# Optimization experiments

Hardware: AMD Instinct MI355X
Metric: run time of the kernel (lower is better)

Reference implementation:

```python
import jax, jax.numpy as jnp
import numpy as np

IMAGE_SIZE = 224
FMAP_H = FMAP_W = 26   # resnet18 layer2 (28x28) after AvgPool2d(3, stride=1)
N_REWEIGHT = 3
SIGMA = 4.0
KSIZE = 2 * int(4.0 * SIGMA + 0.5) + 1  # 33, kornia-style default kernel for sigma=4


def _gaussian_kernel1d():
    x = np.arange(KSIZE, dtype=np.float64) - (KSIZE - 1) / 2.0
    k = np.exp(-0.5 * (x / SIGMA) ** 2)
    return jnp.asarray((k / k.sum()).astype(np.float32))


def _cdist(x, y):
    # Euclidean cdist: x [N,D], y [M,D] -> [N,M], via the expanded quadratic form.
    x2 = jnp.sum(x * x, axis=1, keepdims=True)          # [N,1]
    y2 = jnp.sum(y * y, axis=1)                          # [M]
    d2 = x2 + y2 - 2.0 * (x @ y.T)                       # [N,M]
    return jnp.sqrt(jnp.maximum(d2, 0.0))


def _gaussian_blur(img):
    # Separable depthwise gaussian blur with reflect padding, img [1,1,H,W].
    k1d = _gaussian_kernel1d()
    pad = (KSIZE - 1) // 2
    x = jnp.pad(img, ((0, 0), (0, 0), (pad, pad), (pad, pad)), mode='reflect')
    kh = k1d.reshape(1, 1, KSIZE, 1)
    kw = k1d.reshape(1, 1, 1, KSIZE)
    dn = ('NCHW', 'OIHW', 'NCHW')
    x = jax.lax.conv_general_dilated(x, kh, (1, 1), 'VALID', dimension_numbers=dn)
    x = jax.lax.conv_general_dilated(x, kw, (1, 1), 'VALID', dimension_numbers=dn)
    return x


def setup_inputs() -> dict:
    key = jax.random.key(0)
    k1, k2 = jax.random.split(key)
    patch = jax.random.normal(k1, (FMAP_H * FMAP_W, 384), dtype=jnp.float32)      # [676, 384]
    patch_lib = jax.random.normal(k2, (100000, 384), dtype=jnp.float32)            # coreset bank
    return {"patch": patch, "patch_lib": patch_lib}


def reference(patch, patch_lib):
    # dist = torch.cdist(patch, patch_lib); min over memory bank
    dist = _cdist(patch, patch_lib)                      # [N, M]
    min_val = jnp.min(dist, axis=1)                      # [N]
    min_idx = jnp.argmin(dist, axis=1)                   # [N]
    s_idx = jnp.argmax(min_val)                          # most anomalous patch
    s_star = min_val[s_idx]
    m_test = patch[s_idx]                                # [D]
    m_star = patch_lib[min_idx[s_idx]]                   # [D]
    # reweighting: k nearest neighbors of m_star in the bank (smallest distances)
    w_dist = jnp.linalg.norm(m_star[None, :] - patch_lib, axis=1)   # [M]
    _, nn_idx = jax.lax.top_k(-w_dist, N_REWEIGHT)                  # indices of k smallest
    m_star_knn = jnp.linalg.norm(m_test[None, :] - patch_lib[nn_idx[1:]], axis=1)  # [k-1]
    D = jnp.sqrt(jnp.asarray(patch.shape[1], dtype=jnp.float32))
    w = 1.0 - jnp.exp(s_star / D) / jnp.sum(jnp.exp(m_star_knn / D))
    s = w * s_star
    # segmentation map: reshape, bilinear upsample (align_corners=False), gaussian blur
    s_map = min_val.reshape(1, 1, FMAP_H, FMAP_W)
    s_map = jax.image.resize(s_map, (1, 1, IMAGE_SIZE, IMAGE_SIZE), method='bilinear')
    s_map = _gaussian_blur(s_map)
    return s, s_map
```

## Files before the change

### kernel.cpp

```cpp
#include <hip/hip_runtime.h>

#define M_PATCH 676
#define K_DIM   384
#define N_LIB   100000
#define BM      128
#define BN      128
#define NCH     782
#define MTILES  6
#define M_PAD   (MTILES*BM)
#define N_PAD   (NCH*BN)
#define XCHUNK  98
#define GRID_GEMM (8*XCHUNK*MTILES)
#define NTOPB   1563
#define NCAND   (NTOPB*3)
#define IMG     224
#define FMAP    26
#define KS      33
#define KHALF   16

typedef __attribute__((ext_vector_type(4))) float  f32x4;
typedef __attribute__((ext_vector_type(8))) short  short8;
typedef unsigned long long ull;

static __device__ __forceinline__ unsigned short f2bf(float f) {
  unsigned u = __float_as_uint(f);
  u = u + 0x7FFFu + ((u >> 16) & 1u);
  return (unsigned short)(u >> 16);
}

static __device__ __forceinline__ ull shfl_xor_u64(ull v, int m) {
  unsigned lo = (unsigned)v, hi = (unsigned)(v >> 32);
  lo = __shfl_xor(lo, m, 64);
  hi = __shfl_xor(hi, m, 64);
  return ((ull)hi << 32) | lo;
}

static __device__ __forceinline__ ull umin64(ull a, ull b) { return a < b ? a : b; }
static __device__ __forceinline__ ull umax64(ull a, ull b) { return a > b ? a : b; }

static __device__ __forceinline__ void gld16(const unsigned short* g, unsigned short* l) {
  __builtin_amdgcn_global_load_lds(
      (const __attribute__((address_space(1))) void*)g,
      (__attribute__((address_space(3))) void*)l, 16, 0, 0);
}

__global__ void pc_norms_cvt_kernel(const float* __restrict__ patch, const float* __restrict__ lib,
                                    float* __restrict__ y2, float* __restrict__ x2,
                                    unsigned short* __restrict__ Abf, unsigned short* __restrict__ Bbf) {
  const int w = threadIdx.x >> 6, lane = threadIdx.x & 63;
  const long r = (long)blockIdx.x * 4 + w;
  if (r < N_PAD) {
    float s;
    if (r < N_LIB) {
      const float2* p = (const float2*)(lib + r * K_DIM);
      ushort2* q = (ushort2*)(Bbf + r * K_DIM);
      float2 v[3];
      s = 0.f;
      #pragma unroll
      for (int j = 0; j < 3; ++j) { v[j] = p[lane + 64 * j]; s += v[j].x * v[j].x + v[j].y * v[j].y; }
      #pragma unroll
      for (int j = 0; j < 3; ++j) q[lane + 64 * j] = make_ushort2(f2bf(v[j].x), f2bf(v[j].y));
      #pragma unroll
      for (int m = 1; m < 64; m <<= 1) s += __shfl_xor(s, m, 64);
    } else {
      s = __builtin_inff();
      ushort2* q = (ushort2*)(Bbf + r * K_DIM);
      #pragma unroll
      for (int j = 0; j < 3; ++j) q[lane + 64 * j] = make_ushort2(0, 0);
    }
    if (lane == 0) y2[r] = s;
  } else {
    const long pr = r - N_PAD;
    if (pr < M_PATCH) {
      const float2* p = (const float2*)(patch + pr * K_DIM);
      ushort2* q = (ushort2*)(Abf + pr * K_DIM);
      float2 v[3]; float s = 0.f;
      #pragma unroll
      for (int j = 0; j < 3; ++j) { v[j] = p[lane + 64 * j]; s += v[j].x * v[j].x + v[j].y * v[j].y; }
      #pragma unroll
      for (int j = 0; j < 3; ++j) q[lane + 64 * j] = make_ushort2(f2bf(v[j].x), f2bf(v[j].y));
      #pragma unroll
      for (int m = 1; m < 64; m <<= 1) s += __shfl_xor(s, m, 64);
      if (lane == 0) x2[pr] = s;
    } else if (pr < M_PAD) {
      ushort2* q = (ushort2*)(Abf + pr * K_DIM);
      #pragma unroll
      for (int j = 0; j < 3; ++j) q[lane + 64 * j] = make_ushort2(0, 0);
    }
  }
}

__launch_bounds__(256, 4)
__global__ void pc_gemm_min_bf16_kernel(const unsigned short* __restrict__ Abf,
                                        const unsigned short* __restrict__ Bbf,
                                        const float* __restrict__ x2g, const float* __restrict__ y2g,
                                        ull* __restrict__ partial) {
  __shared__ unsigned short As[2][BM * 32];
  __shared__ unsigned short Bs[2][BN * 32];
  __shared__ float x2s[BM];
  __shared__ float y2s[BN];
  __shared__ ull red[BM * 2];

  const int l = blockIdx.x;
  const int xcd = l & 7, slot = l >> 3;
  const int chunk = xcd * XCHUNK + slot / MTILES;
  const int mtile = slot % MTILES;
  if (chunk >= NCH) return;

  const int t = threadIdx.x;
  const int m0 = mtile * BM;
  const int n0 = chunk * BN;
  const int wid = t >> 6, lane = t & 63;

  if (t < BM) {
    const int gm = m0 + t;
    x2s[t] = (gm < M_PATCH) ? x2g[gm] : 0.f;
    y2s[t] = y2g[n0 + t];
  }

  const int srow   = (wid << 4) + (lane >> 2);
  const int spiece = (lane & 3) ^ ((lane >> 4) & 3);
  const unsigned short* gA0 = Abf + (size_t)(m0 + srow) * K_DIM + spiece * 8;
  const unsigned short* gA1 = gA0 + (size_t)64 * K_DIM;
  const unsigned short* gB0 = Bbf + (size_t)(n0 + srow) * K_DIM + spiece * 8;
  const unsigned short* gB1 = gB0 + (size_t)64 * K_DIM;

  f32x4 acc[4][4];
  #pragma unroll
  for (int i = 0; i < 4; ++i)
    #pragma unroll
    for (int j = 0; j < 4; ++j) acc[i][j] = (f32x4){0.f, 0.f, 0.f, 0.f};

  const int wm = wid >> 1, wn = wid & 1;
  const int quad = lane >> 4, l15 = lane & 15;
  const int poff = (quad ^ ((l15 >> 2) & 3)) * 8;

  for (int ks = 0; ks < K_DIM / 64; ++ks) {
    __syncthreads();
    #pragma unroll
    for (int h = 0; h < 2; ++h) {
      const int ko = ks * 64 + h * 32;
      gld16(gA0 + ko, &As[h][wid * 512]);
      gld16(gA1 + ko, &As[h][(wid + 4) * 512]);
      gld16(gB0 + ko, &Bs[h][wid * 512]);
      gld16(gB1 + ko, &Bs[h][(wid + 4) * 512]);
    }
    __builtin_amdgcn_s_waitcnt(0);
    __syncthreads();

    #pragma unroll
    for (int h = 0; h < 2; ++h) {
      short8 af[4], bf[4];
      #pragma unroll
      for (int mi = 0; mi < 4; ++mi)
        af[mi] = *(const short8*)&As[h][(wm * 64 + mi * 16 + l15) * 32 + poff];
      #pragma unroll
      for (int ni = 0; ni < 4; ++ni)
        bf[ni] = *(const short8*)&Bs[h][(wn * 64 + ni * 16 + l15) * 32 + poff];
      #pragma unroll
      for (int mi = 0; mi < 4; ++mi)
        #pragma unroll
        for (int ni = 0; ni < 4; ++ni)
          acc[mi][ni] = __builtin_amdgcn_mfma_f32_16x16x32_bf16(af[mi], bf[ni], acc[mi][ni], 0, 0, 0);
    }
  }

  #pragma unroll
  for (int mi = 0; mi < 4; ++mi) {
    #pragma unroll
    for (int r = 0; r < 4; ++r) {
      const int row_l = wm * 64 + mi * 16 + quad * 4 + r;
      const float xs = x2s[row_l];
      ull kmin = ~0ull;
      #pragma unroll
      for (int ni = 0; ni < 4; ++ni) {
        const int col_l = wn * 64 + ni * 16 + l15;
        float d2 = xs + y2s[col_l] - 2.0f * acc[mi][ni][r];
        d2 = fmaxf(d2, 0.0f);
        const ull key = ((ull)__float_as_uint(d2) << 32) | (unsigned)(n0 + col_l);
        kmin = umin64(kmin, key);
      }
      #pragma unroll
      for (int off = 1; off < 16; off <<= 1) kmin = umin64(kmin, shfl_xor_u64(kmin, off));
      if (l15 == 0) red[row_l * 2 + wn] = kmin;
    }
  }
  __syncthreads();
  if (t < BM) {
    const ull k = umin64(red[t * 2], red[t * 2 + 1]);
    partial[(size_t)chunk * M_PAD + m0 + t] = k;
  }
}

__global__ void pc_reduce_kernel(const ull* __restrict__ partial,
                                 float* __restrict__ minval, unsigned* __restrict__ minidx) {
  const int m = blockIdx.x;
  const int t = threadIdx.x;
  ull k = ~0ull;
  for (int c = t; c < NCH; c += 128) k = umin64(k, partial[(size_t)c * M_PAD + m]);
  #pragma unroll
  for (int off = 1; off < 64; off <<= 1) k = umin64(k, shfl_xor_u64(k, off));
  __shared__ ull sh[2];
  if ((t & 63) == 0) sh[t >> 6] = k;
  __syncthreads();
  if (t == 0) {
    k = umin64(sh[0], sh[1]);
    const float d2 = __uint_as_float((unsigned)(k >> 32));
    minval[m] = sqrtf(fmaxf(d2, 0.f));
    minidx[m] = (unsigned)k;
  }
}

__global__ void pc_select_kernel(const float* __restrict__ minval, const unsigned* __restrict__ minidx,
                                 unsigned* __restrict__ scal) {
  const int t = threadIdx.x;
  ull k = 0ull;
  for (int m = t; m < M_PATCH; m += 256) {
    const ull key = ((ull)__float_as_uint(minval[m]) << 32) | (0xFFFFFFFFu - (unsigned)m);
    k = umax64(k, key);
  }
  #pragma unroll
  for (int off = 1; off < 64; off <<= 1) k = umax64(k, shfl_xor_u64(k, off));
  __shared__ ull sh[4];
  if ((t & 63) == 0) sh[t >> 6] = k;
  __syncthreads();
  if (t == 0) {
    #pragma unroll
    for (int w = 1; w < 4; ++w) k = umax64(k, sh[w]);
    const unsigned m = 0xFFFFFFFFu - (unsigned)k;
    scal[0] = m;
    scal[1] = (unsigned)(k >> 32);
    scal[2] = minidx[m];
  }
}

__global__ void pc_wdist_top3_kernel(const float* __restrict__ lib, const unsigned* __restrict__ scal,
                                     ull* __restrict__ cand) {
  __shared__ ull keys[64];
  const int t = threadIdx.x, w = t >> 6, lane = t & 63;
  const float2* ms = (const float2*)(lib + (size_t)scal[2] * K_DIM);
  float2 msv[3];
  #pragma unroll
  for (int j = 0; j < 3; ++j) msv[j] = ms[lane + 64 * j];
  const long r0 = (long)blockIdx.x * 64 + w * 16;
  for (int i = 0; i < 16; ++i) {
    const long r = r0 + i;
    ull key = ~0ull;
    if (r < N_LIB) {
      const float2* p = (const float2*)(lib + r * K_DIM);
      float s = 0.f;
      #pragma unroll
      for (int j = 0; j < 3; ++j) {
        const float2 v = p[lane + 64 * j];
        const float dx = v.x - msv[j].x, dy = v.y - msv[j].y;
        s += dx * dx + dy * dy;
      }
      #pragma unroll
      for (int m = 1; m < 64; m <<= 1) s += __shfl_xor(s, m, 64);
      key = ((ull)__float_as_uint(s) << 32) | (unsigned)r;
    }
    if (lane == 0) keys[w * 16 + i] = key;
  }
  __syncthreads();
  if (t == 0) {
    ull picks[3];
    #pragma unroll
    for (int p = 0; p < 3; ++p) {
      ull best = ~0ull;
      for (int i = 0; i < 64; ++i) {
        const ull k = keys[i];
        if ((p > 0 && k == picks[0]) || (p > 1 && k == picks[1])) continue;
        best = umin64(best, k);
      }
      picks[p] = best;
      cand[(long)blockIdx.x * 3 + p] = best;
    }
  }
}

__global__ void pc_top3_merge_kernel(const ull* __restrict__ cand, unsigned* __restrict__ scal) {
  __shared__ ull shm[16];
  __shared__ ull picks_s[3];
  const int t = threadIdx.x;
  for (int p = 0; p < 3; ++p) {
    const ull e0 = (p > 0) ? picks_s[0] : 0ull;
    const ull e1 = (p > 1) ? picks_s[1] : 0ull;
    ull k = ~0ull;
    for (int n = t; n < NCAND; n += 1024) {
      const ull c = cand[n];
      if ((p > 0 && c == e0) || (p > 1 && c == e1)) continue;
      k = umin64(k, c);
    }
    #pragma unroll
    for (int off = 1; off < 64; off <<= 1) k = umin64(k, shfl_xor_u64(k, off));
    if ((t & 63) == 0) shm[t >> 6] = k;
    __syncthreads();
    if (t == 0) {
      #pragma unroll
      for (int w = 1; w < 16; ++w) k = umin64(k, shm[w]);
      picks_s[p] = k;
    }
    __syncthreads();
  }
  if (t == 0) { scal[3] = (unsigned)picks_s[1]; scal[4] = (unsigned)picks_s[2]; }
}

__global__ void pc_final_kernel(const float* __restrict__ patch, const float* __restrict__ lib,
                                const unsigned* __restrict__ scal, float* __restrict__ out) {
  const int w = threadIdx.x >> 6, lane = threadIdx.x & 63;
  __shared__ float sh[2];
  const unsigned nn = scal[3 + w];
  const float* mt = patch + (long)scal[0] * K_DIM;
  const float* pv = lib + (long)nn * K_DIM;
  float s = 0.f;
  #pragma unroll
  for (int j = 0; j < 6; ++j) { const float d = mt[lane + 64 * j] - pv[lane + 64 * j]; s += d * d; }
  #pragma unroll
  for (int m = 1; m < 64; m <<= 1) s += __shfl_xor(s, m, 64);
  if (lane == 0) sh[w] = s;
  __syncthreads();
  if (threadIdx.x == 0) {
    const float D = sqrtf((float)K_DIM);
    const float s_star = __uint_as_float(scal[1]);
    const float a = sqrtf(sh[0]), b = sqrtf(sh[1]);
    const float wgt = 1.f - expf(s_star / D) / (expf(a / D) + expf(b / D));
    out[0] = wgt * s_star;
  }
}

__global__ void pc_upsample_kernel(const float* __restrict__ mv, float* __restrict__ up) {
  const int idx = blockIdx.x * 256 + threadIdx.x;
  if (idx >= IMG * IMG) return;
  const int y = idx / IMG, x = idx - y * IMG;
  const float scale = (float)FMAP / (float)IMG;
  const float fy = ((float)y + 0.5f) * scale - 0.5f;
  const float fx = ((float)x + 0.5f) * scale - 0.5f;
  const int iy0 = (int)floorf(fy); const float ty = fy - (float)iy0;
  const int ix0 = (int)floorf(fx); const float tx = fx - (float)ix0;
  const int y0 = min(max(iy0, 0), FMAP - 1), y1 = min(max(iy0 + 1, 0), FMAP - 1);
  const int x0 = min(max(ix0, 0), FMAP - 1), x1 = min(max(ix0 + 1, 0), FMAP - 1);
  const float v00 = mv[y0 * FMAP + x0], v01 = mv[y0 * FMAP + x1];
  const float v10 = mv[y1 * FMAP + x0], v11 = mv[y1 * FMAP + x1];
  const float v0 = v00 + (v01 - v00) * tx;
  const float v1 = v10 + (v11 - v10) * tx;
  up[idx] = v0 + (v1 - v0) * ty;
}

static __device__ __forceinline__ int pc_refl(int i) {
  return i < 0 ? -i : (i >= IMG ? 2 * IMG - 2 - i : i);
}

__global__ void pc_blur_kernel(const float* __restrict__ src, float* __restrict__ dst, int along_x) {
  __shared__ double kd[KS];
  __shared__ double ksum;
  __shared__ float kf[KS];
  const int t = threadIdx.x;
  if (t < KS) { const double xx = (double)(t - KHALF) / 4.0; kd[t] = exp(-0.5 * xx * xx); }
  __syncthreads();
  if (t == 0) { double s = 0.0; for (int i = 0; i < KS; ++i) s += kd[i]; ksum = s; }
  __syncthreads();
  if (t < KS) kf[t] = (float)(kd[t] / ksum);
  __syncthreads();
  const int idx = blockIdx.x * 256 + t;
  if (idx >= IMG * IMG) return;
  const int y = idx / IMG, x = idx - y * IMG;
  float s = 0.f;
  if (along_x) {
    #pragma unroll
    for (int i = 0; i < KS; ++i) s += kf[i] * src[y * IMG + pc_refl(x + i - KHALF)];
  } else {
    #pragma unroll
    for (int i = 0; i < KS; ++i) s += kf[i] * src[pc_refl(y + i - KHALF) * IMG + x];
  }
  dst[idx] = s;
}

extern "C" void kernel_launch(void* const* d_in, const int* in_sizes, int n_in,
                              void* d_out, int out_size, void* d_ws, size_t ws_size,
                              hipStream_t stream) {
  const float* patch = (const float*)d_in[0];
  const float* lib   = (const float*)d_in[1];
  float* out = (float*)d_out;

  char* p = (char*)d_ws;
  auto take = [&](size_t n) { char* q = p; p += (n + 511) & ~(size_t)511; return q; };
  float* y2        = (float*)take((size_t)N_PAD * 4);
  float* x2        = (float*)take((size_t)M_PAD * 4);
  ull* partial     = (ull*)take((size_t)NCH * M_PAD * 8);
  float* minval    = (float*)take((size_t)M_PATCH * 4);
  unsigned* minidx = (unsigned*)take((size_t)M_PATCH * 4);
  unsigned* scal   = (unsigned*)take(64);
  ull* cand        = (ull*)take((size_t)NCAND * 8);
  float* up        = (float*)take((size_t)IMG * IMG * 4);
  float* tmpb      = (float*)take((size_t)IMG * IMG * 4);
  unsigned short* Abf = (unsigned short*)take((size_t)M_PAD * K_DIM * 2);
  unsigned short* Bbf = (unsigned short*)take((size_t)N_PAD * K_DIM * 2);
  (void)in_sizes; (void)n_in; (void)out_size; (void)ws_size;

  const int norm_rows = N_PAD + M_PAD;
  pc_norms_cvt_kernel<<<(norm_rows + 3) / 4, 256, 0, stream>>>(patch, lib, y2, x2, Abf, Bbf);

  pc_gemm_min_bf16_kernel<<<GRID_GEMM, 256, 0, stream>>>(Abf, Bbf, x2, y2, partial);

  pc_reduce_kernel<<<M_PATCH, 128, 0, stream>>>(partial, minval, minidx);
  pc_select_kernel<<<1, 256, 0, stream>>>(minval, minidx, scal);
  pc_wdist_top3_kernel<<<NTOPB, 256, 0, stream>>>(lib, scal, cand);
  pc_top3_merge_kernel<<<1, 1024, 0, stream>>>(cand, scal);
  pc_final_kernel<<<1, 128, 0, stream>>>(patch, lib, scal, out);

  pc_upsample_kernel<<<(IMG * IMG + 255) / 256, 256, 0, stream>>>(minval, up);
  pc_blur_kernel<<<(IMG * IMG + 255) / 256, 256, 0, stream>>>(up, tmpb, 0);
  pc_blur_kernel<<<(IMG * IMG + 255) / 256, 256, 0, stream>>>(tmpb, out + 1, 1);
}
```

Baseline: 386.8 us.

## Pre-swizzle operands into MFMA fragment layout and fuse tail kernels

The conversion kernel now writes bf16 operands already arranged in MFMA fragment order, so the GEMM reads fragments straight from global memory without LDS staging or barriers. Launch bounds drop from 4 to 3. The reduce, select, top-3 merge and final steps are merged with last-block-done atomic counters, and upsample plus both blur passes are fused into one per-row kernel. This removes several launches, the LDS round trip in the GEMM and intermediate image buffers. In exchange the GEMM depends on global/L2 latency without software pipelining, the memsets add small cost, and the reduce assumes the partial buffer is padded to 784 chunks.

```diff
diff --git a/kernel.cpp b/kernel.cpp
--- a/kernel.cpp
+++ b/kernel.cpp
@@ -9,10 +9,13 @@
 #define MTILES  6
 #define M_PAD   (MTILES*BM)
 #define N_PAD   (NCH*BN)
+#define NBG     (N_PAD/16)
+#define NAG     (M_PAD/16)
 #define XCHUNK  98
 #define GRID_GEMM (8*XCHUNK*MTILES)
 #define NTOPB   1563
 #define NCAND   (NTOPB*3)
+#define SH_LD   392
 #define IMG     224
 #define FMAP    26
 #define KS      33
@@ -38,65 +41,65 @@
 static __device__ __forceinline__ ull umin64(ull a, ull b) { return a < b ? a : b; }
 static __device__ __forceinline__ ull umax64(ull a, ull b) { return a > b ? a : b; }
 
-static __device__ __forceinline__ void gld16(const unsigned short* g, unsigned short* l) {
-  __builtin_amdgcn_global_load_lds(
-      (const __attribute__((address_space(1))) void*)g,
-      (__attribute__((address_space(3))) void*)l, 16, 0, 0);
-}
-
-__global__ void pc_norms_cvt_kernel(const float* __restrict__ patch, const float* __restrict__ lib,
-                                    float* __restrict__ y2, float* __restrict__ x2,
-                                    unsigned short* __restrict__ Abf, unsigned short* __restrict__ Bbf) {
-  const int w = threadIdx.x >> 6, lane = threadIdx.x & 63;
-  const long r = (long)blockIdx.x * 4 + w;
-  if (r < N_PAD) {
-    float s;
-    if (r < N_LIB) {
-      const float2* p = (const float2*)(lib + r * K_DIM);
-      ushort2* q = (ushort2*)(Bbf + r * K_DIM);
-      float2 v[3];
-      s = 0.f;
-      #pragma unroll
-      for (int j = 0; j < 3; ++j) { v[j] = p[lane + 64 * j]; s += v[j].x * v[j].x + v[j].y * v[j].y; }
-      #pragma unroll
-      for (int j = 0; j < 3; ++j) q[lane + 64 * j] = make_ushort2(f2bf(v[j].x), f2bf(v[j].y));
-      #pragma unroll
-      for (int m = 1; m < 64; m <<= 1) s += __shfl_xor(s, m, 64);
-    } else {
-      s = __builtin_inff();
-      ushort2* q = (ushort2*)(Bbf + r * K_DIM);
-      #pragma unroll
-      for (int j = 0; j < 3; ++j) q[lane + 64 * j] = make_ushort2(0, 0);
-    }
-    if (lane == 0) y2[r] = s;
-  } else {
-    const long pr = r - N_PAD;
-    if (pr < M_PATCH) {
-      const float2* p = (const float2*)(patch + pr * K_DIM);
-      ushort2* q = (ushort2*)(Abf + pr * K_DIM);
-      float2 v[3]; float s = 0.f;
-      #pragma unroll
-      for (int j = 0; j < 3; ++j) { v[j] = p[lane + 64 * j]; s += v[j].x * v[j].x + v[j].y * v[j].y; }
-      #pragma unroll
-      for (int j = 0; j < 3; ++j) q[lane + 64 * j] = make_ushort2(f2bf(v[j].x), f2bf(v[j].y));
-      #pragma unroll
-      for (int m = 1; m < 64; m <<= 1) s += __shfl_xor(s, m, 64);
-      if (lane == 0) x2[pr] = s;
-    } else if (pr < M_PAD) {
-      ushort2* q = (ushort2*)(Abf + pr * K_DIM);
-      #pragma unroll
-      for (int j = 0; j < 3; ++j) q[lane + 64 * j] = make_ushort2(0, 0);
-    }
-  }
-}
-
-__launch_bounds__(256, 4)
-__global__ void pc_gemm_min_bf16_kernel(const unsigned short* __restrict__ Abf,
-                                        const unsigned short* __restrict__ Bbf,
-                                        const float* __restrict__ x2g, const float* __restrict__ y2g,
-                                        ull* __restrict__ partial) {
-  __shared__ unsigned short As[2][BM * 32];
-  __shared__ unsigned short Bs[2][BN * 32];
+__global__ void pc_cvt_kernel(const float* __restrict__ patch, const float* __restrict__ lib,
+                              float* __restrict__ y2, float* __restrict__ x2,
+                              unsigned short* __restrict__ Afrag, unsigned short* __restrict__ Bfrag) {
+  __shared__ unsigned short sh[16 * SH_LD];
+  const int t = threadIdx.x;
+  const int g = blockIdx.x;
+  const bool isB = (g < NBG);
+  const int gl = isB ? g : (g - NBG);
+  const long r0 = (long)gl * 16;
+  const float* src = isB ? lib : patch;
+  const int nrows = isB ? N_LIB : M_PATCH;
+
+  #pragma unroll
+  for (int i = 0; i < 6; ++i) {
+    const int f = i * 256 + t;
+    const int r = f / 96, c = f - r * 96;
+    const long gr = r0 + r;
+    float4 v = make_float4(0.f, 0.f, 0.f, 0.f);
+    if (gr < nrows) v = ((const float4*)(src + (size_t)gr * K_DIM))[c];
+    *(ushort4*)&sh[r * SH_LD + c * 4] = make_ushort4(f2bf(v.x), f2bf(v.y), f2bf(v.z), f2bf(v.w));
+  }
+  __syncthreads();
+
+  const int w = t >> 6, lane = t & 63;
+  #pragma unroll
+  for (int q = 0; q < 4; ++q) {
+    const int r = w * 4 + q;
+    float s = 0.f;
+    #pragma unroll
+    for (int j = 0; j < 6; ++j) {
+      const float v = __uint_as_float((unsigned)sh[r * SH_LD + lane + 64 * j] << 16);
+      s += v * v;
+    }
+    #pragma unroll
+    for (int m = 1; m < 64; m <<= 1) s += __shfl_xor(s, m, 64);
+    if (lane == 0) {
+      const long gr = r0 + r;
+      if (isB) y2[r0 + r] = (gr < N_LIB) ? s : __builtin_inff();
+      else     x2[r0 + r] = s;
+    }
+  }
+
+  unsigned short* dst = isB ? (Bfrag + (size_t)gl * 12 * 512)
+                            : (Afrag + (size_t)gl * 12 * 512);
+  #pragma unroll
+  for (int i = 0; i < 3; ++i) {
+    const int c2 = i * 256 + t;
+    const int kt = c2 >> 6, ln = c2 & 63;
+    const int srow = ln & 15, koff = kt * 32 + (ln >> 4) * 8;
+    const short8 vv = *(const short8*)&sh[srow * SH_LD + koff];
+    *(short8*)&dst[(size_t)kt * 512 + ln * 8] = vv;
+  }
+}
+
+__launch_bounds__(256, 3)
+__global__ void pc_gemm_min_kernel(const unsigned short* __restrict__ Afrag,
+                                   const unsigned short* __restrict__ Bfrag,
+                                   const float* __restrict__ x2g, const float* __restrict__ y2g,
+                                   ull* __restrict__ partial) {
   __shared__ float x2s[BM];
   __shared__ float y2s[BN];
   __shared__ ull red[BM * 2];
@@ -111,6 +114,7 @@
   const int m0 = mtile * BM;
   const int n0 = chunk * BN;
   const int wid = t >> 6, lane = t & 63;
+  const int wm = wid >> 1, wn = wid & 1;
 
   if (t < BM) {
     const int gm = m0 + t;
@@ -118,12 +122,8 @@
     y2s[t] = y2g[n0 + t];
   }
 
-  const int srow   = (wid << 4) + (lane >> 2);
-  const int spiece = (lane & 3) ^ ((lane >> 4) & 3);
-  const unsigned short* gA0 = Abf + (size_t)(m0 + srow) * K_DIM + spiece * 8;
-  const unsigned short* gA1 = gA0 + (size_t)64 * K_DIM;
-  const unsigned short* gB0 = Bbf + (size_t)(n0 + srow) * K_DIM + spiece * 8;
-  const unsigned short* gB1 = gB0 + (size_t)64 * K_DIM;
+  const unsigned short* Ab = Afrag + (size_t)(mtile * 8 + wm * 4) * 12 * 512 + lane * 8;
+  const unsigned short* Bb = Bfrag + (size_t)(chunk * 8 + wn * 4) * 12 * 512 + lane * 8;
 
   f32x4 acc[4][4];
   #pragma unroll
@@ -131,40 +131,25 @@
     #pragma unroll
     for (int j = 0; j < 4; ++j) acc[i][j] = (f32x4){0.f, 0.f, 0.f, 0.f};
 
-  const int wm = wid >> 1, wn = wid & 1;
+  #pragma unroll 2
+  for (int ks = 0; ks < 12; ++ks) {
+    short8 af[4], bf[4];
+    #pragma unroll
+    for (int mi = 0; mi < 4; ++mi)
+      af[mi] = *(const short8*)(Ab + ((size_t)mi * 12 + ks) * 512);
+    #pragma unroll
+    for (int ni = 0; ni < 4; ++ni)
+      bf[ni] = *(const short8*)(Bb + ((size_t)ni * 12 + ks) * 512);
+    #pragma unroll
+    for (int mi = 0; mi < 4; ++mi)
+      #pragma unroll
+      for (int ni = 0; ni < 4; ++ni)
+        acc[mi][ni] = __builtin_amdgcn_mfma_f32_16x16x32_bf16(af[mi], bf[ni], acc[mi][ni], 0, 0, 0);
+  }
+
+  __syncthreads();
+
   const int quad = lane >> 4, l15 = lane & 15;
-  const int poff = (quad ^ ((l15 >> 2) & 3)) * 8;
-
-  for (int ks = 0; ks < K_DIM / 64; ++ks) {
-    __syncthreads();
-    #pragma unroll
-    for (int h = 0; h < 2; ++h) {
-      const int ko = ks * 64 + h * 32;
-      gld16(gA0 + ko, &As[h][wid * 512]);
-      gld16(gA1 + ko, &As[h][(wid + 4) * 512]);
-      gld16(gB0 + ko, &Bs[h][wid * 512]);
-      gld16(gB1 + ko, &Bs[h][(wid + 4) * 512]);
-    }
-    __builtin_amdgcn_s_waitcnt(0);
-    __syncthreads();
-
-    #pragma unroll
-    for (int h = 0; h < 2; ++h) {
-      short8 af[4], bf[4];
-      #pragma unroll
-      for (int mi = 0; mi < 4; ++mi)
-        af[mi] = *(const short8*)&As[h][(wm * 64 + mi * 16 + l15) * 32 + poff];
-      #pragma unroll
-      for (int ni = 0; ni < 4; ++ni)
-        bf[ni] = *(const short8*)&Bs[h][(wn * 64 + ni * 16 + l15) * 32 + poff];
-      #pragma unroll
-      for (int mi = 0; mi < 4; ++mi)
-        #pragma unroll
-        for (int ni = 0; ni < 4; ++ni)
-          acc[mi][ni] = __builtin_amdgcn_mfma_f32_16x16x32_bf16(af[mi], bf[ni], acc[mi][ni], 0, 0, 0);
-    }
-  }
-
   #pragma unroll
   for (int mi = 0; mi < 4; ++mi) {
     #pragma unroll
@@ -192,50 +177,52 @@
   }
 }
 
-__global__ void pc_reduce_kernel(const ull* __restrict__ partial,
-                                 float* __restrict__ minval, unsigned* __restrict__ minidx) {
-  const int m = blockIdx.x;
+__global__ void pc_reduce_kernel(const ull* __restrict__ partial, ull* __restrict__ stage1,
+                                 float* __restrict__ minval, unsigned* __restrict__ minidx,
+                                 unsigned* __restrict__ scal) {
+  const int b = blockIdx.x, mt = b >> 3, gp = b & 7;
   const int t = threadIdx.x;
+  const int c0 = gp * XCHUNK;
   ull k = ~0ull;
-  for (int c = t; c < NCH; c += 128) k = umin64(k, partial[(size_t)c * M_PAD + m]);
-  #pragma unroll
-  for (int off = 1; off < 64; off <<= 1) k = umin64(k, shfl_xor_u64(k, off));
+  #pragma unroll 7
+  for (int i = 0; i < XCHUNK; ++i)
+    k = umin64(k, partial[(size_t)(c0 + i) * M_PAD + mt * 128 + t]);
+  stage1[(size_t)(mt * 128 + t) * 8 + gp] = k;
+  __threadfence();
+  __syncthreads();
+  __shared__ unsigned rank_s;
+  if (t == 0) rank_s = atomicAdd(&scal[8], 1u);
+  __syncthreads();
+  if (rank_s != 47) return;
+  __threadfence();
+
+  ull best = 0ull;
+  for (int m = t; m < M_PATCH; m += 128) {
+    ull kk = ~0ull;
+    #pragma unroll
+    for (int g = 0; g < 8; ++g) kk = umin64(kk, stage1[(size_t)m * 8 + g]);
+    const float d = sqrtf(fmaxf(__uint_as_float((unsigned)(kk >> 32)), 0.f));
+    minval[m] = d;
+    minidx[m] = (unsigned)kk;
+    best = umax64(best, ((ull)__float_as_uint(d) << 32) | (0xFFFFFFFFu - (unsigned)m));
+  }
+  #pragma unroll
+  for (int off = 1; off < 64; off <<= 1) best = umax64(best, shfl_xor_u64(best, off));
   __shared__ ull sh[2];
-  if ((t & 63) == 0) sh[t >> 6] = k;
+  if ((t & 63) == 0) sh[t >> 6] = best;
   __syncthreads();
   if (t == 0) {
-    k = umin64(sh[0], sh[1]);
-    const float d2 = __uint_as_float((unsigned)(k >> 32));
-    minval[m] = sqrtf(fmaxf(d2, 0.f));
-    minidx[m] = (unsigned)k;
-  }
-}
-
-__global__ void pc_select_kernel(const float* __restrict__ minval, const unsigned* __restrict__ minidx,
-                                 unsigned* __restrict__ scal) {
-  const int t = threadIdx.x;
-  ull k = 0ull;
-  for (int m = t; m < M_PATCH; m += 256) {
-    const ull key = ((ull)__float_as_uint(minval[m]) << 32) | (0xFFFFFFFFu - (unsigned)m);
-    k = umax64(k, key);
-  }
-  #pragma unroll
-  for (int off = 1; off < 64; off <<= 1) k = umax64(k, shfl_xor_u64(k, off));
-  __shared__ ull sh[4];
-  if ((t & 63) == 0) sh[t >> 6] = k;
-  __syncthreads();
-  if (t == 0) {
-    #pragma unroll
-    for (int w = 1; w < 4; ++w) k = umax64(k, sh[w]);
-    const unsigned m = 0xFFFFFFFFu - (unsigned)k;
+    best = umax64(sh[0], sh[1]);
+    const unsigned m = 0xFFFFFFFFu - (unsigned)best;
     scal[0] = m;
-    scal[1] = (unsigned)(k >> 32);
+    scal[1] = (unsigned)(best >> 32);
     scal[2] = minidx[m];
   }
 }
 
-__global__ void pc_wdist_top3_kernel(const float* __restrict__ lib, const unsigned* __restrict__ scal,
-                                     ull* __restrict__ cand) {
+__global__ void pc_wdist_kernel(const float* __restrict__ patch, const float* __restrict__ lib,
+                                unsigned* __restrict__ scal, ull* __restrict__ cand,
+                                float* __restrict__ out) {
   __shared__ ull keys[64];
   const int t = threadIdx.x, w = t >> 6, lane = t & 63;
   const float2* ms = (const float2*)(lib + (size_t)scal[2] * K_DIM);
@@ -266,27 +253,31 @@
     ull picks[3];
     #pragma unroll
     for (int p = 0; p < 3; ++p) {
-      ull best = ~0ull;
+      ull bestk = ~0ull;
       for (int i = 0; i < 64; ++i) {
         const ull k = keys[i];
         if ((p > 0 && k == picks[0]) || (p > 1 && k == picks[1])) continue;
-        best = umin64(best, k);
+        bestk = umin64(bestk, k);
       }
-      picks[p] = best;
-      cand[(long)blockIdx.x * 3 + p] = best;
-    }
-  }
-}
-
-__global__ void pc_top3_merge_kernel(const ull* __restrict__ cand, unsigned* __restrict__ scal) {
-  __shared__ ull shm[16];
+      picks[p] = bestk;
+      cand[(long)blockIdx.x * 3 + p] = bestk;
+    }
+  }
+  __threadfence();
+  __syncthreads();
+  __shared__ unsigned rank_s;
+  if (t == 0) rank_s = atomicAdd(&scal[9], 1u);
+  __syncthreads();
+  if (rank_s != NTOPB - 1) return;
+  __threadfence();
+
+  __shared__ ull shm[4];
   __shared__ ull picks_s[3];
-  const int t = threadIdx.x;
   for (int p = 0; p < 3; ++p) {
     const ull e0 = (p > 0) ? picks_s[0] : 0ull;
     const ull e1 = (p > 1) ? picks_s[1] : 0ull;
     ull k = ~0ull;
-    for (int n = t; n < NCAND; n += 1024) {
+    for (int n = t; n < NCAND; n += 256) {
       const ull c = cand[n];
       if ((p > 0 && c == e0) || (p > 1 && c == e1)) continue;
       k = umin64(k, c);
@@ -297,82 +288,79 @@
     __syncthreads();
     if (t == 0) {
       #pragma unroll
-      for (int w = 1; w < 16; ++w) k = umin64(k, shm[w]);
+      for (int ww = 1; ww < 4; ++ww) k = umin64(k, shm[ww]);
       picks_s[p] = k;
     }
     __syncthreads();
   }
-  if (t == 0) { scal[3] = (unsigned)picks_s[1]; scal[4] = (unsigned)picks_s[2]; }
-}
-
-__global__ void pc_final_kernel(const float* __restrict__ patch, const float* __restrict__ lib,
-                                const unsigned* __restrict__ scal, float* __restrict__ out) {
-  const int w = threadIdx.x >> 6, lane = threadIdx.x & 63;
-  __shared__ float sh[2];
-  const unsigned nn = scal[3 + w];
-  const float* mt = patch + (long)scal[0] * K_DIM;
-  const float* pv = lib + (long)nn * K_DIM;
-  float s = 0.f;
-  #pragma unroll
-  for (int j = 0; j < 6; ++j) { const float d = mt[lane + 64 * j] - pv[lane + 64 * j]; s += d * d; }
-  #pragma unroll
-  for (int m = 1; m < 64; m <<= 1) s += __shfl_xor(s, m, 64);
-  if (lane == 0) sh[w] = s;
-  __syncthreads();
-  if (threadIdx.x == 0) {
+  __shared__ float sh2[2];
+  if (w < 2) {
+    const unsigned nn = (unsigned)picks_s[1 + w];
+    const float* mt2 = patch + (size_t)scal[0] * K_DIM;
+    const float* pv  = lib + (size_t)nn * K_DIM;
+    float s = 0.f;
+    #pragma unroll
+    for (int j = 0; j < 6; ++j) { const float d = mt2[lane + 64 * j] - pv[lane + 64 * j]; s += d * d; }
+    #pragma unroll
+    for (int m = 1; m < 64; m <<= 1) s += __shfl_xor(s, m, 64);
+    if (lane == 0) sh2[w] = s;
+  }
+  __syncthreads();
+  if (t == 0) {
     const float D = sqrtf((float)K_DIM);
     const float s_star = __uint_as_float(scal[1]);
-    const float a = sqrtf(sh[0]), b = sqrtf(sh[1]);
+    const float a = sqrtf(sh2[0]), b = sqrtf(sh2[1]);
     const float wgt = 1.f - expf(s_star / D) / (expf(a / D) + expf(b / D));
     out[0] = wgt * s_star;
   }
 }
 
-__global__ void pc_upsample_kernel(const float* __restrict__ mv, float* __restrict__ up) {
-  const int idx = blockIdx.x * 256 + threadIdx.x;
-  if (idx >= IMG * IMG) return;
-  const int y = idx / IMG, x = idx - y * IMG;
-  const float scale = (float)FMAP / (float)IMG;
-  const float fy = ((float)y + 0.5f) * scale - 0.5f;
-  const float fx = ((float)x + 0.5f) * scale - 0.5f;
-  const int iy0 = (int)floorf(fy); const float ty = fy - (float)iy0;
-  const int ix0 = (int)floorf(fx); const float tx = fx - (float)ix0;
-  const int y0 = min(max(iy0, 0), FMAP - 1), y1 = min(max(iy0 + 1, 0), FMAP - 1);
-  const int x0 = min(max(ix0, 0), FMAP - 1), x1 = min(max(ix0 + 1, 0), FMAP - 1);
-  const float v00 = mv[y0 * FMAP + x0], v01 = mv[y0 * FMAP + x1];
-  const float v10 = mv[y1 * FMAP + x0], v11 = mv[y1 * FMAP + x1];
-  const float v0 = v00 + (v01 - v00) * tx;
-  const float v1 = v10 + (v11 - v10) * tx;
-  up[idx] = v0 + (v1 - v0) * ty;
-}
-
 static __device__ __forceinline__ int pc_refl(int i) {
   return i < 0 ? -i : (i >= IMG ? 2 * IMG - 2 - i : i);
 }
 
-__global__ void pc_blur_kernel(const float* __restrict__ src, float* __restrict__ dst, int along_x) {
-  __shared__ double kd[KS];
-  __shared__ double ksum;
+__global__ void pc_map_kernel(const float* __restrict__ minval, float* __restrict__ outmap) {
+  __shared__ double kd[KS + 1];
   __shared__ float kf[KS];
+  __shared__ float smap[FMAP * FMAP];
+  __shared__ float by[IMG];
   const int t = threadIdx.x;
+  const int y = blockIdx.x;
   if (t < KS) { const double xx = (double)(t - KHALF) / 4.0; kd[t] = exp(-0.5 * xx * xx); }
-  __syncthreads();
-  if (t == 0) { double s = 0.0; for (int i = 0; i < KS; ++i) s += kd[i]; ksum = s; }
-  __syncthreads();
-  if (t < KS) kf[t] = (float)(kd[t] / ksum);
-  __syncthreads();
-  const int idx = blockIdx.x * 256 + t;
-  if (idx >= IMG * IMG) return;
-  const int y = idx / IMG, x = idx - y * IMG;
-  float s = 0.f;
-  if (along_x) {
-    #pragma unroll
-    for (int i = 0; i < KS; ++i) s += kf[i] * src[y * IMG + pc_refl(x + i - KHALF)];
-  } else {
-    #pragma unroll
-    for (int i = 0; i < KS; ++i) s += kf[i] * src[pc_refl(y + i - KHALF) * IMG + x];
-  }
-  dst[idx] = s;
+  for (int i = t; i < FMAP * FMAP; i += 256) smap[i] = minval[i];
+  __syncthreads();
+  if (t == 0) { double s = 0.0; for (int i = 0; i < KS; ++i) s += kd[i]; kd[KS] = s; }
+  __syncthreads();
+  if (t < KS) kf[t] = (float)(kd[t] / kd[KS]);
+  __syncthreads();
+
+  const float scale = (float)FMAP / (float)IMG;
+  if (t < IMG) {
+    const float fx = ((float)t + 0.5f) * scale - 0.5f;
+    const int ix0 = (int)floorf(fx); const float tx = fx - (float)ix0;
+    const int x0 = min(max(ix0, 0), FMAP - 1), x1 = min(max(ix0 + 1, 0), FMAP - 1);
+    float s = 0.f;
+    #pragma unroll
+    for (int j = 0; j < KS; ++j) {
+      const int yy = pc_refl(y + j - KHALF);
+      const float fy = ((float)yy + 0.5f) * scale - 0.5f;
+      const int iy0 = (int)floorf(fy); const float ty = fy - (float)iy0;
+      const int y0 = min(max(iy0, 0), FMAP - 1), y1 = min(max(iy0 + 1, 0), FMAP - 1);
+      const float v00 = smap[y0 * FMAP + x0], v01 = smap[y0 * FMAP + x1];
+      const float v10 = smap[y1 * FMAP + x0], v11 = smap[y1 * FMAP + x1];
+      const float v0 = v00 + (v01 - v00) * tx;
+      const float v1 = v10 + (v11 - v10) * tx;
+      s += kf[j] * (v0 + (v1 - v0) * ty);
+    }
+    by[t] = s;
+  }
+  __syncthreads();
+  if (t < IMG) {
+    float s = 0.f;
+    #pragma unroll
+    for (int i = 0; i < KS; ++i) s += kf[i] * by[pc_refl(t + i - KHALF)];
+    outmap[y * IMG + t] = s;
+  }
 }
 
 extern "C" void kernel_launch(void* const* d_in, const int* in_sizes, int n_in,
@@ -386,29 +374,22 @@
   auto take = [&](size_t n) { char* q = p; p += (n + 511) & ~(size_t)511; return q; };
   float* y2        = (float*)take((size_t)N_PAD * 4);
   float* x2        = (float*)take((size_t)M_PAD * 4);
-  ull* partial     = (ull*)take((size_t)NCH * M_PAD * 8);
+  ull* partial     = (ull*)take((size_t)(NCH + 2) * M_PAD * 8);
+  ull* stage1      = (ull*)take((size_t)M_PAD * 8 * 8);
   float* minval    = (float*)take((size_t)M_PATCH * 4);
   unsigned* minidx = (unsigned*)take((size_t)M_PATCH * 4);
-  unsigned* scal   = (unsigned*)take(64);
+  unsigned* scal   = (unsigned*)take(256);
   ull* cand        = (ull*)take((size_t)NCAND * 8);
-  float* up        = (float*)take((size_t)IMG * IMG * 4);
-  float* tmpb      = (float*)take((size_t)IMG * IMG * 4);
-  unsigned short* Abf = (unsigned short*)take((size_t)M_PAD * K_DIM * 2);
-  unsigned short* Bbf = (unsigned short*)take((size_t)N_PAD * K_DIM * 2);
+  unsigned short* Afrag = (unsigned short*)take((size_t)NAG * 12 * 512 * 2);
+  unsigned short* Bfrag = (unsigned short*)take((size_t)NBG * 12 * 512 * 2);
   (void)in_sizes; (void)n_in; (void)out_size; (void)ws_size;
 
-  const int norm_rows = N_PAD + M_PAD;
-  pc_norms_cvt_kernel<<<(norm_rows + 3) / 4, 256, 0, stream>>>(patch, lib, y2, x2, Abf, Bbf);
-
-  pc_gemm_min_bf16_kernel<<<GRID_GEMM, 256, 0, stream>>>(Abf, Bbf, x2, y2, partial);
-
-  pc_reduce_kernel<<<M_PATCH, 128, 0, stream>>>(partial, minval, minidx);
-  pc_select_kernel<<<1, 256, 0, stream>>>(minval, minidx, scal);
-  pc_wdist_top3_kernel<<<NTOPB, 256, 0, stream>>>(lib, scal, cand);
-  pc_top3_merge_kernel<<<1, 1024, 0, stream>>>(cand, scal);
-  pc_final_kernel<<<1, 128, 0, stream>>>(patch, lib, scal, out);
-
-  pc_upsample_kernel<<<(IMG * IMG + 255) / 256, 256, 0, stream>>>(minval, up);
-  pc_blur_kernel<<<(IMG * IMG + 255) / 256, 256, 0, stream>>>(up, tmpb, 0);
-  pc_blur_kernel<<<(IMG * IMG + 255) / 256, 256, 0, stream>>>(tmpb, out + 1, 1);
-}
+  hipMemsetAsync(scal, 0, 64, stream);
+  hipMemsetAsync(partial + (size_t)NCH * M_PAD, 0xFF, 2 * M_PAD * 8, stream);
+
+  pc_cvt_kernel<<<NBG + NAG, 256, 0, stream>>>(patch, lib, y2, x2, Afrag, Bfrag);
+  pc_gemm_min_kernel<<<GRID_GEMM, 256, 0, stream>>>(Afrag, Bfrag, x2, y2, partial);
+  pc_reduce_kernel<<<48, 128, 0, stream>>>(partial, stage1, minval, minidx, scal);
+  pc_wdist_kernel<<<NTOPB, 256, 0, stream>>>(patch, lib, scal, cand, out);
+  pc_map_kernel<<<IMG, 256, 0, stream>>>(minval, out + 1);
+}
```

New measurement: 508.6 us. +31.5%, slower.
